# Optimization experiments

Measured on AMD Instinct MI355X. Metric: run time of the kernel, lower is better.

The kernel has to match this reference:

```python
import jax, jax.numpy as jnp
import numpy as np

B, S, D, H = 2, 2048, 1024, 16
DK = D // H


def setup_inputs() -> dict:
    key = jax.random.key(0)
    ks = jax.random.split(key, 12)
    std = 1.0 / np.sqrt(D)
    inp = {
        "query": jax.random.normal(ks[0], (B, S, D), jnp.float32),
        "key": jax.random.normal(ks[1], (B, S, D), jnp.float32),
        "value": jax.random.normal(ks[2], (B, S, D), jnp.float32),
        # causal mask: 1 = keep, 0 = blocked (matches masked_fill(mask==0, -inf))
        "mask": jnp.tril(jnp.ones((S, S), jnp.int32))[None, None, :, :],
        # torch Linear convention: W is (out, in), y = x @ W.T + b
        "Wq": jax.random.normal(ks[3], (D, D), jnp.float32) * std,
        "bq": jax.random.normal(ks[4], (D,), jnp.float32) * std,
        "Wk": jax.random.normal(ks[5], (D, D), jnp.float32) * std,
        "bk": jax.random.normal(ks[6], (D,), jnp.float32) * std,
        "Wv": jax.random.normal(ks[7], (D, D), jnp.float32) * std,
        "bv": jax.random.normal(ks[8], (D,), jnp.float32) * std,
        "Wo": jax.random.normal(ks[9], (D, D), jnp.float32) * std,
        "bo": jax.random.normal(ks[10], (D,), jnp.float32) * std,
    }
    return inp


def reference(query, key, value, mask, Wq, bq, Wk, bk, Wv, bv, Wo, bo):
    b = query.shape[0]
    # projections (torch Linear: x @ W.T + b)
    Q = query @ Wq.T + bq
    K = key @ Wk.T + bk
    V = value @ Wv.T + bv
    # (b, s, d) -> (b, h, s, dk)
    Q = Q.reshape(b, -1, H, DK).transpose(0, 2, 1, 3)
    K = K.reshape(b, -1, H, DK).transpose(0, 2, 1, 3)
    V = V.reshape(b, -1, H, DK).transpose(0, 2, 1, 3)
    scores = jnp.einsum("bhqd,bhkd->bhqk", Q, K) / jnp.sqrt(jnp.float32(DK))
    scores = jnp.where(mask == 0, -jnp.inf, scores)
    weights = jax.nn.softmax(scores, axis=-1)  # dropout p=0.0 / eval mode: no-op
    attn = jnp.einsum("bhqk,bhkd->bhqd", weights, V)
    attn = attn.transpose(0, 2, 1, 3).reshape(b, -1, D)
    return attn @ Wo.T + bo
```

## Files before the change

kernel.cpp:

```cpp
#include <hip/hip_runtime.h>
#include <hip/hip_bf16.h>
#include <cstdint>
#include <cstddef>


#define B_ 2
#define S_ 2048
#define D_ 1024
#define H_ 16
#define DK_ 64
#define QSCALE 0.1803368801111244f

typedef __attribute__((ext_vector_type(8))) short bf16x8;
typedef __attribute__((ext_vector_type(4))) float f32x4;
typedef __attribute__((ext_vector_type(16))) float f32x16;
typedef __attribute__((ext_vector_type(4))) unsigned short u16x4;
typedef __attribute__((ext_vector_type(4))) float float4v;
typedef __attribute__((ext_vector_type(2))) unsigned int u32x2;
typedef __attribute__((ext_vector_type(4))) unsigned int u32x4;

__device__ __forceinline__ unsigned short f2bf(float f) {
  unsigned int u = __float_as_uint(f);
  u += 0x7FFFu + ((u >> 16) & 1u);
  return (unsigned short)(u >> 16);
}
__device__ __forceinline__ unsigned int cvt_pk_bf16(float lo, float hi) {
  unsigned int r;
  asm("v_cvt_pk_bf16_f32 %0, %1, %2" : "=v"(r) : "v"(lo), "v"(hi));
  return r;
}
__device__ __forceinline__ bf16x8 lds_read_sw64(const unsigned short* base, int row, int col) {
  int P = (row * 64 + col) * 2;
  int X = P ^ ((row & 7) << 4);
  return *(const bf16x8*)((const char*)base + X);
}

__global__ __launch_bounds__(256) void cvt3(const float* __restrict__ s0,
                                            const float* __restrict__ s1,
                                            const float* __restrict__ s2,
                                            unsigned short* __restrict__ d0,
                                            unsigned short* __restrict__ d1,
                                            unsigned short* __restrict__ d2) {
  const float* src = blockIdx.y == 0 ? s0 : blockIdx.y == 1 ? s1 : s2;
  unsigned short* dst = blockIdx.y == 0 ? d0 : blockIdx.y == 1 ? d1 : d2;
  int i = blockIdx.x * 256 + threadIdx.x;
  float4v v = *(const float4v*)(src + (size_t)i * 4);
  u16x4 o;
  o[0] = f2bf(v[0]); o[1] = f2bf(v[1]); o[2] = f2bf(v[2]); o[3] = f2bf(v[3]);
  *(u16x4*)(dst + (size_t)i * 4) = o;
}

__global__ __launch_bounds__(256) void cvt4(const float* __restrict__ s0,
                                            const float* __restrict__ s1,
                                            const float* __restrict__ s2,
                                            const float* __restrict__ s3,
                                            unsigned short* __restrict__ d0,
                                            unsigned short* __restrict__ d1,
                                            unsigned short* __restrict__ d2,
                                            unsigned short* __restrict__ d3) {
  int z = blockIdx.y;
  const float* src = z == 0 ? s0 : z == 1 ? s1 : z == 2 ? s2 : s3;
  unsigned short* dst = z == 0 ? d0 : z == 1 ? d1 : z == 2 ? d2 : d3;
  int i = blockIdx.x * 256 + threadIdx.x;
  float4v v = *(const float4v*)(src + (size_t)i * 4);
  u16x4 o;
  o[0] = f2bf(v[0]); o[1] = f2bf(v[1]); o[2] = f2bf(v[2]); o[3] = f2bf(v[3]);
  *(u16x4*)(dst + (size_t)i * 4) = o;
}

__global__ __launch_bounds__(256) void gemm_qkv(
    const unsigned short* __restrict__ Xq, const unsigned short* __restrict__ Xk,
    const unsigned short* __restrict__ Xv, const unsigned short* __restrict__ Wq,
    const unsigned short* __restrict__ Wk, const unsigned short* __restrict__ Wv,
    const float* __restrict__ bq, const float* __restrict__ bk,
    const float* __restrict__ bv, unsigned short* __restrict__ Qp,
    unsigned short* __restrict__ Kp, unsigned short* __restrict__ Vt) {
  const int z = blockIdx.z;
  const unsigned short* A = z == 0 ? Xq : z == 1 ? Xk : Xv;
  const unsigned short* W = z == 0 ? Wq : z == 1 ? Wk : Wv;
  const float* bias = z == 0 ? bq : z == 1 ? bk : bv;
  const int K = D_, N = D_;

  __shared__ __align__(16) unsigned short As[128 * 64];
  __shared__ __align__(16) unsigned short Bs[128 * 64];
  const int tid  = threadIdx.x;
  const int lane = tid & 63;
  const int m0 = blockIdx.x * 128;
  const int n0 = blockIdx.y * 128;
  const int wr = ((tid >> 6) >> 1) * 64;
  const int wc = ((tid >> 6) & 1) * 64;
  const int lr = lane & 15;
  const int lk = (lane >> 4) * 8;
  f32x4 acc[4][4] = {};

  int dstX[4], srow[4], scolu[4];
#pragma unroll
  for (int i = 0; i < 4; ++i) {
    int X = tid * 16 + i * 4096;
    int P = X ^ (((X >> 7) & 7) << 4);
    dstX[i] = X;
    srow[i] = P >> 7;
    scolu[i] = (P & 127) >> 1;
  }

  for (int k0 = 0; k0 < K; k0 += 64) {
    __syncthreads();
#pragma unroll
    for (int i = 0; i < 4; ++i) {
      const unsigned short* gA = A + (size_t)(m0 + srow[i]) * K + k0 + scolu[i];
      const unsigned short* gB = W + (size_t)(n0 + srow[i]) * K + k0 + scolu[i];
      __builtin_amdgcn_global_load_lds((const __attribute__((address_space(1))) void*)gA,
          (__attribute__((address_space(3))) void*)((char*)As + dstX[i]), 16, 0, 0);
      __builtin_amdgcn_global_load_lds((const __attribute__((address_space(1))) void*)gB,
          (__attribute__((address_space(3))) void*)((char*)Bs + dstX[i]), 16, 0, 0);
    }
    __syncthreads();
#pragma unroll
    for (int kk = 0; kk < 2; ++kk) {
      bf16x8 a[4], b[4];
#pragma unroll
      for (int m = 0; m < 4; ++m)
        a[m] = lds_read_sw64(As, wr + m * 16 + lr, kk * 32 + lk);
#pragma unroll
      for (int n = 0; n < 4; ++n)
        b[n] = lds_read_sw64(Bs, wc + n * 16 + lr, kk * 32 + lk);
#pragma unroll
      for (int m = 0; m < 4; ++m)
#pragma unroll
        for (int n = 0; n < 4; ++n)
          acc[m][n] = __builtin_amdgcn_mfma_f32_16x16x32_bf16(a[m], b[n], acc[m][n], 0, 0, 0);
    }
  }

  const int rbase = (lane >> 4) * 4;
  if (z == 2) {
#pragma unroll
    for (int m = 0; m < 4; ++m)
#pragma unroll
      for (int n = 0; n < 4; ++n) {
        int col = n0 + wc + n * 16 + lr;
        float bvv = bias[col];
        int row0 = m0 + wr + m * 16 + rbase;
        int bb = row0 >> 11, s = row0 & 2047;
        int h = col >> 6, dk = col & 63;
        u16x4 o;
#pragma unroll
        for (int r = 0; r < 4; ++r) o[r] = f2bf(acc[m][n][r] + bvv);
        size_t idx = (((size_t)bb * H_ + h) * DK_ + dk) * S_ + s;
        *(u16x4*)(Vt + idx) = o;
      }
  } else {
    unsigned short* Cout = z == 0 ? Qp : Kp;
    const float scale = z == 0 ? QSCALE : 1.0f;
#pragma unroll
    for (int m = 0; m < 4; ++m)
#pragma unroll
      for (int n = 0; n < 4; ++n) {
        int col = n0 + wc + n * 16 + lr;
        float bvv = bias[col];
#pragma unroll
        for (int r = 0; r < 4; ++r) {
          int row = m0 + wr + m * 16 + rbase + r;
          Cout[(size_t)row * N + col] = f2bf((acc[m][n][r] + bvv) * scale);
        }
      }
  }
}

__global__ __launch_bounds__(256) void gemm_o(const unsigned short* __restrict__ A,
                                              const unsigned short* __restrict__ W,
                                              const float* __restrict__ bias,
                                              float* __restrict__ C,
                                              int M, int N, int K) {
  __shared__ __align__(16) unsigned short As[64 * 64];
  __shared__ __align__(16) unsigned short Bs[128 * 64];
  const int tid  = threadIdx.x;
  const int lane = tid & 63;
  const int m0 = blockIdx.x * 64;
  const int n0 = blockIdx.y * 128;
  const int wr = ((tid >> 6) >> 1) * 32;
  const int wc = ((tid >> 6) & 1) * 64;
  const int lr = lane & 15;
  const int lk = (lane >> 4) * 8;
  f32x4 acc[2][4] = {};

  int dstX[4], srow[4], scolu[4];
#pragma unroll
  for (int i = 0; i < 4; ++i) {
    int X = tid * 16 + i * 4096;
    int P = X ^ (((X >> 7) & 7) << 4);
    dstX[i] = X;
    srow[i] = P >> 7;
    scolu[i] = (P & 127) >> 1;
  }

  for (int k0 = 0; k0 < K; k0 += 64) {
    __syncthreads();
#pragma unroll
    for (int i = 0; i < 2; ++i) {
      const unsigned short* gA = A + (size_t)(m0 + srow[i]) * K + k0 + scolu[i];
      __builtin_amdgcn_global_load_lds((const __attribute__((address_space(1))) void*)gA,
          (__attribute__((address_space(3))) void*)((char*)As + dstX[i]), 16, 0, 0);
    }
#pragma unroll
    for (int i = 0; i < 4; ++i) {
      const unsigned short* gB = W + (size_t)(n0 + srow[i]) * K + k0 + scolu[i];
      __builtin_amdgcn_global_load_lds((const __attribute__((address_space(1))) void*)gB,
          (__attribute__((address_space(3))) void*)((char*)Bs + dstX[i]), 16, 0, 0);
    }
    __syncthreads();
#pragma unroll
    for (int kk = 0; kk < 2; ++kk) {
      bf16x8 a[2], b[4];
#pragma unroll
      for (int m = 0; m < 2; ++m)
        a[m] = lds_read_sw64(As, wr + m * 16 + lr, kk * 32 + lk);
#pragma unroll
      for (int n = 0; n < 4; ++n)
        b[n] = lds_read_sw64(Bs, wc + n * 16 + lr, kk * 32 + lk);
#pragma unroll
      for (int m = 0; m < 2; ++m)
#pragma unroll
        for (int n = 0; n < 4; ++n)
          acc[m][n] = __builtin_amdgcn_mfma_f32_16x16x32_bf16(a[m], b[n], acc[m][n], 0, 0, 0);
    }
  }

  const int rbase = (lane >> 4) * 4;
#pragma unroll
  for (int m = 0; m < 2; ++m)
#pragma unroll
    for (int n = 0; n < 4; ++n) {
      int col = n0 + wc + n * 16 + lr;
      float bvv = bias[col];
#pragma unroll
      for (int r = 0; r < 4; ++r) {
        int row = m0 + wr + m * 16 + rbase + r;
        C[(size_t)row * N + col] = acc[m][n][r] + bvv;
      }
    }
}

__device__ __forceinline__ bf16x8 lds_read_swK(const unsigned short* base, int row, int col) {
  int P = (row * 64 + col) * 2;
  int X = P ^ ((row & 7) << 4);
  return *(const bf16x8*)((const char*)base + X);
}
__device__ __forceinline__ bf16x8 lds_read_swV(const unsigned short* base, int row, int col) {
  int P = (row * 128 + col) * 2;
  int X = P ^ ((row & 7) << 4);
  return *(const bf16x8*)((const char*)base + X);
}

__global__ __launch_bounds__(512, 4) void flash_attn(const unsigned short* __restrict__ Qp,
                                                     const unsigned short* __restrict__ Kp,
                                                     const unsigned short* __restrict__ Vtp,
                                                     unsigned short* __restrict__ Op) {
  __shared__ __align__(16) unsigned short smem[32768];

  const int tid  = threadIdx.x;
  const int lane = tid & 63;
  const int w = tid >> 6;
  const int qh = w & 1;
  const int kq = w >> 1;
  const int h  = blockIdx.y;
  const int b  = blockIdx.z;
  const int ql = lane & 31;
  const int hi5 = lane >> 5;
  const size_t basebs = (size_t)b * S_ * D_;
  const int hoff = h * DK_;

  const unsigned short* gK0 = Kp + basebs + hoff;
  const unsigned short* gV0 = Vtp + ((size_t)b * H_ + h) * DK_ * S_;

  int dstXK[2], srcK[2], srcV[2];
#pragma unroll
  for (int i = 0; i < 2; ++i) {
    int X = tid * 16 + i * 8192;
    int Pk = X ^ (((X >> 7) & 7) << 4);
    dstXK[i] = X;
    srcK[i] = (Pk >> 7) * D_ + ((Pk & 127) >> 1);
    int Pv = X ^ (((X >> 8) & 7) << 4);
    srcV[i] = (Pv >> 8) * S_ + ((Pv & 255) >> 1);
  }

#define STAGE(RR, BUF)                                                         \
  {                                                                            \
    const unsigned short* gK = gK0 + (size_t)((RR) * 128) * D_;                \
    const unsigned short* gV = gV0 + (RR) * 128;                               \
    char* kb = (char*)smem + (BUF) * 32768;                                    \
    char* vb = kb + 16384;                                                     \
    _Pragma("unroll")                                                          \
    for (int i = 0; i < 2; ++i) {                                              \
      __builtin_amdgcn_global_load_lds(                                        \
          (const __attribute__((address_space(1))) void*)(gK + srcK[i]),       \
          (__attribute__((address_space(3))) void*)(kb + dstXK[i]), 16, 0, 0); \
      __builtin_amdgcn_global_load_lds(                                        \
          (const __attribute__((address_space(1))) void*)(gV + srcV[i]),       \
          (__attribute__((address_space(3))) void*)(vb + dstXK[i]), 16, 0, 0); \
    }                                                                          \
  }

  for (int s = 0; s < 2; ++s) {
    const int qt = s == 0 ? 31 - (int)blockIdx.x : (int)blockIdx.x;
    const int q0 = qt * 64;
    const int qbase = q0 + qh * 32;
    const int qglob = qbase + ql;

    bf16x8 qf[4];
    {
      const unsigned short* qrow = Qp + basebs + (size_t)qglob * D_ + hoff;
#pragma unroll
      for (int f = 0; f < 4; ++f)
        qf[f] = *(const bf16x8*)(qrow + f * 16 + hi5 * 8);
    }

    float m_r = -1e30f;
    float l_r = 0.f;
    f32x16 out0 = {};
    f32x16 out1 = {};

    const int R = (qt + 2) >> 1;

    STAGE(0, 0);
    __syncthreads();

    for (int r = 0; r < R; ++r) {
      const int cur = r & 1;
      if (r + 1 < R) STAGE(r + 1, cur ^ 1);

      const unsigned short* Kb = smem + cur * 16384;
      const unsigned short* Vb = Kb + 8192;

      const int kv0w = r * 128 + kq * 32;
      const bool act = (kv0w <= qbase);
      const bool part = (kv0w == qbase);

      if (act) {
        f32x16 sc = {};
        __builtin_amdgcn_s_setprio(1);
#pragma unroll
        for (int f = 0; f < 4; ++f) {
          bf16x8 kf = lds_read_swK(Kb, kq * 32 + ql, f * 16 + hi5 * 8);
          sc = __builtin_amdgcn_mfma_f32_32x32x16_bf16(kf, qf[f], sc, 0, 0, 0);
        }
        __builtin_amdgcn_s_setprio(0);

        if (part) {
#pragma unroll
          for (int g = 0; g < 16; ++g) {
            int kvg = kv0w + (g & 3) + 8 * (g >> 2) + 4 * hi5;
            if (kvg > qglob) sc[g] = -1e30f;
          }
        }

        float pm = sc[0];
#pragma unroll
        for (int g = 1; g < 16; ++g) pm = fmaxf(pm, sc[g]);
        pm = fmaxf(pm, __shfl_xor(pm, 32));

        if (!__all(pm - m_r <= 8.0f)) {
          float mnew = fmaxf(m_r, pm);
          float scl = __builtin_exp2f(m_r - mnew);
          l_r *= scl;
#pragma unroll
          for (int g = 0; g < 16; ++g) { out0[g] *= scl; out1[g] *= scl; }
          m_r = mnew;
        }

        float l_add = 0.f;
#define PV_CHUNK(HALF)                                                         \
        {                                                                      \
          const int g0 = (HALF) * 8;                                           \
          float p0 = __builtin_exp2f(sc[g0 + 0] - m_r);                        \
          float p1 = __builtin_exp2f(sc[g0 + 1] - m_r);                        \
          float p2 = __builtin_exp2f(sc[g0 + 2] - m_r);                        \
          float p3 = __builtin_exp2f(sc[g0 + 3] - m_r);                        \
          float p4 = __builtin_exp2f(sc[g0 + 4] - m_r);                        \
          float p5 = __builtin_exp2f(sc[g0 + 5] - m_r);                        \
          float p6 = __builtin_exp2f(sc[g0 + 6] - m_r);                        \
          float p7 = __builtin_exp2f(sc[g0 + 7] - m_r);                        \
          l_add += ((p0 + p1) + (p2 + p3)) + ((p4 + p5) + (p6 + p7));          \
          unsigned int u0 = cvt_pk_bf16(p0, p1);                               \
          unsigned int u1 = cvt_pk_bf16(p2, p3);                               \
          unsigned int u2 = cvt_pk_bf16(p4, p5);                               \
          unsigned int u3 = cvt_pk_bf16(p6, p7);                               \
          unsigned int ta = hi5 ? u0 : u2, tb = hi5 ? u1 : u3;                 \
          unsigned int ra = (unsigned int)__shfl_xor((int)ta, 32);             \
          unsigned int rb = (unsigned int)__shfl_xor((int)tb, 32);             \
          u32x4 pw = {hi5 ? ra : u0, hi5 ? rb : u1,                            \
                      hi5 ? u2 : ra, hi5 ? u3 : rb};                           \
          bf16x8 pf = __builtin_bit_cast(bf16x8, pw);                          \
          int vcol = kq * 32 + (HALF) * 16 + hi5 * 8;                          \
          bf16x8 vf0 = lds_read_swV(Vb, ql, vcol);                             \
          out0 = __builtin_amdgcn_mfma_f32_32x32x16_bf16(vf0, pf, out0, 0, 0, 0);\
          bf16x8 vf1 = lds_read_swV(Vb, 32 + ql, vcol);                       \
          out1 = __builtin_amdgcn_mfma_f32_32x32x16_bf16(vf1, pf, out1, 0, 0, 0);\
        }
        __builtin_amdgcn_s_setprio(1);
        PV_CHUNK(0);
        PV_CHUNK(1);
        __builtin_amdgcn_s_setprio(0);
#undef PV_CHUNK

        l_add += __shfl_xor(l_add, 32);
        l_r += l_add;
      }
      __syncthreads();
    }

    float* scr = (float*)smem;
    if (kq != 0) {
      float* p = scr + (((size_t)qh * 3 + (kq - 1)) * 64 + lane) * 34;
#pragma unroll
      for (int g = 0; g < 16; ++g) { p[g] = out0[g]; p[16 + g] = out1[g]; }
      p[32] = m_r;
      p[33] = l_r;
    }
    __syncthreads();
    if (kq == 0) {
      float mA = m_r, lA = l_r;
#pragma unroll
      for (int j = 0; j < 3; ++j) {
        const float* p = scr + (((size_t)qh * 3 + j) * 64 + lane) * 34;
        float mj = p[32], lj = p[33];
        float mM = fmaxf(mA, mj);
        float s0 = __builtin_exp2f(mA - mM);
        float s1 = __builtin_exp2f(mj - mM);
#pragma unroll
        for (int g = 0; g < 16; ++g) {
          out0[g] = out0[g] * s0 + p[g] * s1;
          out1[g] = out1[g] * s0 + p[16 + g] * s1;
        }
        lA = lA * s0 + lj * s1;
        mA = mM;
      }
      float rcp = 1.0f / lA;
      unsigned short* orow = Op + basebs + (size_t)qglob * D_ + hoff;
#pragma unroll
      for (int i = 0; i < 4; ++i) {
        u32x2 o0 = {cvt_pk_bf16(out0[4 * i + 0] * rcp, out0[4 * i + 1] * rcp),
                    cvt_pk_bf16(out0[4 * i + 2] * rcp, out0[4 * i + 3] * rcp)};
        *(u32x2*)(orow + 8 * i + 4 * hi5) = o0;
        u32x2 o1 = {cvt_pk_bf16(out1[4 * i + 0] * rcp, out1[4 * i + 1] * rcp),
                    cvt_pk_bf16(out1[4 * i + 2] * rcp, out1[4 * i + 3] * rcp)};
        *(u32x2*)(orow + 32 + 8 * i + 4 * hi5) = o1;
      }
    }
    __syncthreads();
  }
#undef STAGE
}

extern "C" void kernel_launch(void* const* d_in, const int* in_sizes, int n_in,
                              void* d_out, int out_size, void* d_ws, size_t ws_size,
                              hipStream_t stream) {
  const float* q  = (const float*)d_in[0];
  const float* k  = (const float*)d_in[1];
  const float* v  = (const float*)d_in[2];
  const float* Wq = (const float*)d_in[4];
  const float* bq = (const float*)d_in[5];
  const float* Wk = (const float*)d_in[6];
  const float* bk = (const float*)d_in[7];
  const float* Wv = (const float*)d_in[8];
  const float* bv = (const float*)d_in[9];
  const float* Wo = (const float*)d_in[10];
  const float* bo = (const float*)d_in[11];

  const int MSD = B_ * S_;
  unsigned short* ws = (unsigned short*)d_ws;
  unsigned short* Xq  = ws;
  unsigned short* Xk  = Xq  + (size_t)MSD * D_;
  unsigned short* Xv  = Xk  + (size_t)MSD * D_;
  unsigned short* Wqb = Xv  + (size_t)MSD * D_;
  unsigned short* Wkb = Wqb + (size_t)D_ * D_;
  unsigned short* Wvb = Wkb + (size_t)D_ * D_;
  unsigned short* Wob = Wvb + (size_t)D_ * D_;
  unsigned short* Qp  = Wob + (size_t)D_ * D_;
  unsigned short* Kp  = Qp  + (size_t)MSD * D_;
  unsigned short* Vt  = Kp  + (size_t)MSD * D_;
  unsigned short* At  = Vt  + (size_t)MSD * D_;

  const int n4a = MSD * D_ / 4;
  const int n4w = D_ * D_ / 4;
  dim3 g3(n4a / 256, 3);
  cvt3<<<g3, 256, 0, stream>>>(q, k, v, Xq, Xk, Xv);
  dim3 g4(n4w / 256, 4);
  cvt4<<<g4, 256, 0, stream>>>(Wq, Wk, Wv, Wo, Wqb, Wkb, Wvb, Wob);

  dim3 gqkv(MSD / 128, D_ / 128, 3);
  gemm_qkv<<<gqkv, 256, 0, stream>>>(Xq, Xk, Xv, Wqb, Wkb, Wvb,
                                     bq, bk, bv, Qp, Kp, Vt);

  dim3 ga(16, H_, B_);
  flash_attn<<<ga, 512, 0, stream>>>(Qp, Kp, Vt, At);

  dim3 go(MSD / 64, D_ / 128);
  gemm_o<<<go, 256, 0, stream>>>(At, Wob, bo, (float*)d_out, MSD, D_, D_);
}
```

Before: 133.2 us.

## Write Q/K/V in MFMA fragment layout and load attention operands directly to registers

The QKV projection epilogue now writes Q, K and V into a per-head fragment-ordered layout, so each lane of the attention kernel can load its MFMA operands with contiguous 16-byte global loads. The attention kernel drops LDS staging, double buffering and per-tile barriers: each of four waves walks its own strided set of 32-row KV tiles, and only the final cross-wave merge uses shared memory. Cross-half shuffles become permlane32_swap, and the grid changes to 32-query blocks of 256 threads. The risk is that K/V reuse across waves now depends on cache rather than LDS, and the Q/K epilogue writes scattered 2-byte stores.

Result: no change. 133.3 us (+0.0%).

```diff
diff --git a/kernel.cpp b/kernel.cpp
--- a/kernel.cpp
+++ b/kernel.cpp
@@ -18,6 +18,7 @@
 typedef __attribute__((ext_vector_type(4))) float float4v;
 typedef __attribute__((ext_vector_type(2))) unsigned int u32x2;
 typedef __attribute__((ext_vector_type(4))) unsigned int u32x4;
+typedef __attribute__((ext_vector_type(2))) int i32x2;
 
 __device__ __forceinline__ unsigned short f2bf(float f) {
   unsigned int u = __float_as_uint(f);
@@ -28,6 +29,15 @@
   unsigned int r;
   asm("v_cvt_pk_bf16_f32 %0, %1, %2" : "=v"(r) : "v"(lo), "v"(hi));
   return r;
+}
+__device__ __forceinline__ float partner32f(float x, int hi5) {
+  int xi = __float_as_int(x);
+  i32x2 r = __builtin_amdgcn_permlane32_swap(xi, xi, false, false);
+  return __int_as_float(hi5 ? r[0] : r[1]);
+}
+__device__ __forceinline__ unsigned int partner32u(unsigned int x, int hi5) {
+  i32x2 r = __builtin_amdgcn_permlane32_swap((int)x, (int)x, false, false);
+  return (unsigned int)(hi5 ? r[0] : r[1]);
 }
 __device__ __forceinline__ bf16x8 lds_read_sw64(const unsigned short* base, int row, int col) {
   int P = (row * 64 + col) * 2;
@@ -73,13 +83,13 @@
     const unsigned short* __restrict__ Xv, const unsigned short* __restrict__ Wq,
     const unsigned short* __restrict__ Wk, const unsigned short* __restrict__ Wv,
     const float* __restrict__ bq, const float* __restrict__ bk,
-    const float* __restrict__ bv, unsigned short* __restrict__ Qp,
-    unsigned short* __restrict__ Kp, unsigned short* __restrict__ Vt) {
+    const float* __restrict__ bv, unsigned short* __restrict__ Qf,
+    unsigned short* __restrict__ Kf, unsigned short* __restrict__ Vf) {
   const int z = blockIdx.z;
   const unsigned short* A = z == 0 ? Xq : z == 1 ? Xk : Xv;
   const unsigned short* W = z == 0 ? Wq : z == 1 ? Wk : Wv;
   const float* bias = z == 0 ? bq : z == 1 ? bk : bv;
-  const int K = D_, N = D_;
+  const int K = D_;
 
   __shared__ __align__(16) unsigned short As[128 * 64];
   __shared__ __align__(16) unsigned short Bs[128 * 64];
@@ -141,16 +151,19 @@
         int col = n0 + wc + n * 16 + lr;
         float bvv = bias[col];
         int row0 = m0 + wr + m * 16 + rbase;
-        int bb = row0 >> 11, s = row0 & 2047;
+        int bb = row0 >> 11, sr = row0 & 2047;
         int h = col >> 6, dk = col & 63;
+        int kv32 = sr >> 5, half = (sr >> 4) & 1, hi5p = (sr >> 3) & 1, e0 = sr & 7;
+        int dt = dk >> 5, qlp = dk & 31;
         u16x4 o;
 #pragma unroll
         for (int r = 0; r < 4; ++r) o[r] = f2bf(acc[m][n][r] + bvv);
-        size_t idx = (((size_t)bb * H_ + h) * DK_ + dk) * S_ + s;
-        *(u16x4*)(Vt + idx) = o;
+        size_t idx = ((((size_t)(bb * H_ + h) * 64 + kv32) * 2 + dt) * 2 + half) * 512
+                     + (hi5p * 32 + qlp) * 8 + e0;
+        *(u16x4*)(Vf + idx) = o;
       }
   } else {
-    unsigned short* Cout = z == 0 ? Qp : Kp;
+    unsigned short* Cout = z == 0 ? Qf : Kf;
     const float scale = z == 0 ? QSCALE : 1.0f;
 #pragma unroll
     for (int m = 0; m < 4; ++m)
@@ -158,11 +171,16 @@
       for (int n = 0; n < 4; ++n) {
         int col = n0 + wc + n * 16 + lr;
         float bvv = bias[col];
-#pragma unroll
-        for (int r = 0; r < 4; ++r) {
-          int row = m0 + wr + m * 16 + rbase + r;
-          Cout[(size_t)row * N + col] = f2bf((acc[m][n][r] + bvv) * scale);
-        }
+        int h = col >> 6, dk = col & 63;
+        int f = dk >> 4, hi5p = (dk >> 3) & 1, e = dk & 7;
+        int row0 = m0 + wr + m * 16 + rbase;
+        int bb = row0 >> 11, sr = row0 & 2047;
+        int s32 = sr >> 5, qlp = sr & 31;
+        size_t base = (((size_t)(bb * H_ + h) * 64 + s32) * 4 + f) * 512
+                      + (hi5p * 32 + qlp) * 8 + e;
+#pragma unroll
+        for (int r = 0; r < 4; ++r)
+          Cout[base + (size_t)r * 8] = f2bf((acc[m][n][r] + bvv) * scale);
       }
   }
 }
@@ -241,78 +259,38 @@
     }
 }
 
-__device__ __forceinline__ bf16x8 lds_read_swK(const unsigned short* base, int row, int col) {
-  int P = (row * 64 + col) * 2;
-  int X = P ^ ((row & 7) << 4);
-  return *(const bf16x8*)((const char*)base + X);
-}
-__device__ __forceinline__ bf16x8 lds_read_swV(const unsigned short* base, int row, int col) {
-  int P = (row * 128 + col) * 2;
-  int X = P ^ ((row & 7) << 4);
-  return *(const bf16x8*)((const char*)base + X);
-}
-
-__global__ __launch_bounds__(512, 4) void flash_attn(const unsigned short* __restrict__ Qp,
-                                                     const unsigned short* __restrict__ Kp,
-                                                     const unsigned short* __restrict__ Vtp,
-                                                     unsigned short* __restrict__ Op) {
-  __shared__ __align__(16) unsigned short smem[32768];
+__global__ __launch_bounds__(256, 4) void flash_reg(const unsigned short* __restrict__ Qf,
+                                                    const unsigned short* __restrict__ Kf,
+                                                    const unsigned short* __restrict__ Vf,
+                                                    unsigned short* __restrict__ Op) {
+  __shared__ float scr[3 * 64 * 34];
 
   const int tid  = threadIdx.x;
   const int lane = tid & 63;
-  const int w = tid >> 6;
-  const int qh = w & 1;
-  const int kq = w >> 1;
+  const int kq   = tid >> 6;
+  const int bx = blockIdx.x;
   const int h  = blockIdx.y;
   const int b  = blockIdx.z;
   const int ql = lane & 31;
   const int hi5 = lane >> 5;
+  const int bh = b * H_ + h;
   const size_t basebs = (size_t)b * S_ * D_;
   const int hoff = h * DK_;
 
-  const unsigned short* gK0 = Kp + basebs + hoff;
-  const unsigned short* gV0 = Vtp + ((size_t)b * H_ + h) * DK_ * S_;
-
-  int dstXK[2], srcK[2], srcV[2];
-#pragma unroll
-  for (int i = 0; i < 2; ++i) {
-    int X = tid * 16 + i * 8192;
-    int Pk = X ^ (((X >> 7) & 7) << 4);
-    dstXK[i] = X;
-    srcK[i] = (Pk >> 7) * D_ + ((Pk & 127) >> 1);
-    int Pv = X ^ (((X >> 8) & 7) << 4);
-    srcV[i] = (Pv >> 8) * S_ + ((Pv & 255) >> 1);
-  }
-
-#define STAGE(RR, BUF)                                                         \
-  {                                                                            \
-    const unsigned short* gK = gK0 + (size_t)((RR) * 128) * D_;                \
-    const unsigned short* gV = gV0 + (RR) * 128;                               \
-    char* kb = (char*)smem + (BUF) * 32768;                                    \
-    char* vb = kb + 16384;                                                     \
-    _Pragma("unroll")                                                          \
-    for (int i = 0; i < 2; ++i) {                                              \
-      __builtin_amdgcn_global_load_lds(                                        \
-          (const __attribute__((address_space(1))) void*)(gK + srcK[i]),       \
-          (__attribute__((address_space(3))) void*)(kb + dstXK[i]), 16, 0, 0); \
-      __builtin_amdgcn_global_load_lds(                                        \
-          (const __attribute__((address_space(1))) void*)(gV + srcV[i]),       \
-          (__attribute__((address_space(3))) void*)(vb + dstXK[i]), 16, 0, 0); \
-    }                                                                          \
-  }
+  const unsigned short* Qb = Qf + (size_t)bh * 131072 + lane * 8;
+  const unsigned short* Kb = Kf + (size_t)bh * 131072 + lane * 8;
+  const unsigned short* Vb = Vf + (size_t)bh * 131072 + lane * 8;
 
   for (int s = 0; s < 2; ++s) {
-    const int qt = s == 0 ? 31 - (int)blockIdx.x : (int)blockIdx.x;
-    const int q0 = qt * 64;
-    const int qbase = q0 + qh * 32;
-    const int qglob = qbase + ql;
-
-    bf16x8 qf[4];
+    const int j = s == 0 ? 63 - bx : bx;
+    const int q0 = j * 32;
+    const int qglob = q0 + ql;
+
+    bf16x8 qf4[4];
     {
-      const unsigned short* qrow = Qp + basebs + (size_t)qglob * D_ + hoff;
-#pragma unroll
-      for (int f = 0; f < 4; ++f)
-        qf[f] = *(const bf16x8*)(qrow + f * 16 + hi5 * 8);
+      const unsigned short* qp_ = Qb + (size_t)j * 2048;
+#pragma unroll
+      for (int f = 0; f < 4; ++f) qf4[f] = *(const bf16x8*)(qp_ + f * 512);
     }
 
     float m_r = -1e30f;
@@ -320,98 +298,88 @@
     f32x16 out0 = {};
     f32x16 out1 = {};
 
-    const int R = (qt + 2) >> 1;
-
-    STAGE(0, 0);
-    __syncthreads();
-
-    for (int r = 0; r < R; ++r) {
-      const int cur = r & 1;
-      if (r + 1 < R) STAGE(r + 1, cur ^ 1);
-
-      const unsigned short* Kb = smem + cur * 16384;
-      const unsigned short* Vb = Kb + 8192;
-
-      const int kv0w = r * 128 + kq * 32;
-      const bool act = (kv0w <= qbase);
-      const bool part = (kv0w == qbase);
-
-      if (act) {
-        f32x16 sc = {};
-        __builtin_amdgcn_s_setprio(1);
-#pragma unroll
-        for (int f = 0; f < 4; ++f) {
-          bf16x8 kf = lds_read_swK(Kb, kq * 32 + ql, f * 16 + hi5 * 8);
-          sc = __builtin_amdgcn_mfma_f32_32x32x16_bf16(kf, qf[f], sc, 0, 0, 0);
+    for (int w = kq; w <= j; w += 4) {
+      const unsigned short* kp_ = Kb + (size_t)w * 2048;
+      bf16x8 kf0 = *(const bf16x8*)(kp_);
+      bf16x8 kf1 = *(const bf16x8*)(kp_ + 512);
+      bf16x8 kf2 = *(const bf16x8*)(kp_ + 1024);
+      bf16x8 kf3 = *(const bf16x8*)(kp_ + 1536);
+
+      f32x16 sc = {};
+      __builtin_amdgcn_s_setprio(1);
+      sc = __builtin_amdgcn_mfma_f32_32x32x16_bf16(kf0, qf4[0], sc, 0, 0, 0);
+      sc = __builtin_amdgcn_mfma_f32_32x32x16_bf16(kf1, qf4[1], sc, 0, 0, 0);
+      sc = __builtin_amdgcn_mfma_f32_32x32x16_bf16(kf2, qf4[2], sc, 0, 0, 0);
+      sc = __builtin_amdgcn_mfma_f32_32x32x16_bf16(kf3, qf4[3], sc, 0, 0, 0);
+      __builtin_amdgcn_s_setprio(0);
+
+      const unsigned short* vp_ = Vb + (size_t)w * 2048;
+      bf16x8 vf00 = *(const bf16x8*)(vp_);
+      bf16x8 vf01 = *(const bf16x8*)(vp_ + 512);
+      bf16x8 vf10 = *(const bf16x8*)(vp_ + 1024);
+      bf16x8 vf11 = *(const bf16x8*)(vp_ + 1536);
+
+      if (w == j) {
+#pragma unroll
+        for (int g = 0; g < 16; ++g) {
+          int kvg = w * 32 + (g & 3) + 8 * (g >> 2) + 4 * hi5;
+          if (kvg > qglob) sc[g] = -1e30f;
         }
-        __builtin_amdgcn_s_setprio(0);
-
-        if (part) {
-#pragma unroll
-          for (int g = 0; g < 16; ++g) {
-            int kvg = kv0w + (g & 3) + 8 * (g >> 2) + 4 * hi5;
-            if (kvg > qglob) sc[g] = -1e30f;
-          }
-        }
-
-        float pm = sc[0];
-#pragma unroll
-        for (int g = 1; g < 16; ++g) pm = fmaxf(pm, sc[g]);
-        pm = fmaxf(pm, __shfl_xor(pm, 32));
-
-        if (!__all(pm - m_r <= 8.0f)) {
-          float mnew = fmaxf(m_r, pm);
-          float scl = __builtin_exp2f(m_r - mnew);
-          l_r *= scl;
-#pragma unroll
-          for (int g = 0; g < 16; ++g) { out0[g] *= scl; out1[g] *= scl; }
-          m_r = mnew;
-        }
-
-        float l_add = 0.f;
-#define PV_CHUNK(HALF)                                                         \
-        {                                                                      \
-          const int g0 = (HALF) * 8;                                           \
-          float p0 = __builtin_exp2f(sc[g0 + 0] - m_r);                        \
-          float p1 = __builtin_exp2f(sc[g0 + 1] - m_r);                        \
-          float p2 = __builtin_exp2f(sc[g0 + 2] - m_r);                        \
-          float p3 = __builtin_exp2f(sc[g0 + 3] - m_r);                        \
-          float p4 = __builtin_exp2f(sc[g0 + 4] - m_r);                        \
-          float p5 = __builtin_exp2f(sc[g0 + 5] - m_r);                        \
-          float p6 = __builtin_exp2f(sc[g0 + 6] - m_r);                        \
-          float p7 = __builtin_exp2f(sc[g0 + 7] - m_r);                        \
-          l_add += ((p0 + p1) + (p2 + p3)) + ((p4 + p5) + (p6 + p7));          \
-          unsigned int u0 = cvt_pk_bf16(p0, p1);                               \
-          unsigned int u1 = cvt_pk_bf16(p2, p3);                               \
-          unsigned int u2 = cvt_pk_bf16(p4, p5);                               \
-          unsigned int u3 = cvt_pk_bf16(p6, p7);                               \
-          unsigned int ta = hi5 ? u0 : u2, tb = hi5 ? u1 : u3;                 \
-          unsigned int ra = (unsigned int)__shfl_xor((int)ta, 32);             \
-          unsigned int rb = (unsigned int)__shfl_xor((int)tb, 32);             \
-          u32x4 pw = {hi5 ? ra : u0, hi5 ? rb : u1,                            \
-                      hi5 ? u2 : ra, hi5 ? u3 : rb};                           \
-          bf16x8 pf = __builtin_bit_cast(bf16x8, pw);                          \
-          int vcol = kq * 32 + (HALF) * 16 + hi5 * 8;                          \
-          bf16x8 vf0 = lds_read_swV(Vb, ql, vcol);                             \
-          out0 = __builtin_amdgcn_mfma_f32_32x32x16_bf16(vf0, pf, out0, 0, 0, 0);\
-          bf16x8 vf1 = lds_read_swV(Vb, 32 + ql, vcol);                       \
-          out1 = __builtin_amdgcn_mfma_f32_32x32x16_bf16(vf1, pf, out1, 0, 0, 0);\
-        }
-        __builtin_amdgcn_s_setprio(1);
-        PV_CHUNK(0);
-        PV_CHUNK(1);
-        __builtin_amdgcn_s_setprio(0);
-#undef PV_CHUNK
-
-        l_add += __shfl_xor(l_add, 32);
-        l_r += l_add;
-      }
-      __syncthreads();
-    }
-
-    float* scr = (float*)smem;
+      }
+
+      float pm = sc[0];
+#pragma unroll
+      for (int g = 1; g < 16; ++g) pm = fmaxf(pm, sc[g]);
+      pm = fmaxf(pm, partner32f(pm, hi5));
+
+      if (!__all(pm - m_r <= 8.0f)) {
+        float mnew = fmaxf(m_r, pm);
+        float scl = __builtin_exp2f(m_r - mnew);
+        l_r *= scl;
+#pragma unroll
+        for (int g = 0; g < 16; ++g) { out0[g] *= scl; out1[g] *= scl; }
+        m_r = mnew;
+      }
+
+      float l_add = 0.f;
+#define PV_HALF(HALF, VF0, VF1)                                                \
+      {                                                                        \
+        const int g0 = (HALF) * 8;                                             \
+        float p0 = __builtin_exp2f(sc[g0 + 0] - m_r);                          \
+        float p1 = __builtin_exp2f(sc[g0 + 1] - m_r);                          \
+        float p2 = __builtin_exp2f(sc[g0 + 2] - m_r);                          \
+        float p3 = __builtin_exp2f(sc[g0 + 3] - m_r);                          \
+        float p4 = __builtin_exp2f(sc[g0 + 4] - m_r);                          \
+        float p5 = __builtin_exp2f(sc[g0 + 5] - m_r);                          \
+        float p6 = __builtin_exp2f(sc[g0 + 6] - m_r);                          \
+        float p7 = __builtin_exp2f(sc[g0 + 7] - m_r);                          \
+        l_add += ((p0 + p1) + (p2 + p3)) + ((p4 + p5) + (p6 + p7));            \
+        unsigned int u0 = cvt_pk_bf16(p0, p1);                                 \
+        unsigned int u1 = cvt_pk_bf16(p2, p3);                                 \
+        unsigned int u2 = cvt_pk_bf16(p4, p5);                                 \
+        unsigned int u3 = cvt_pk_bf16(p6, p7);                                 \
+        unsigned int ta = hi5 ? u0 : u2, tb = hi5 ? u1 : u3;                   \
+        unsigned int ra = partner32u(ta, hi5);                                 \
+        unsigned int rb = partner32u(tb, hi5);                                 \
+        u32x4 pw = {hi5 ? ra : u0, hi5 ? rb : u1,                              \
+                    hi5 ? u2 : ra, hi5 ? u3 : rb};                             \
+        bf16x8 pf = __builtin_bit_cast(bf16x8, pw);                            \
+        out0 = __builtin_amdgcn_mfma_f32_32x32x16_bf16(VF0, pf, out0, 0, 0, 0);\
+        out1 = __builtin_amdgcn_mfma_f32_32x32x16_bf16(VF1, pf, out1, 0, 0, 0);\
+      }
+      __builtin_amdgcn_s_setprio(1);
+      PV_HALF(0, vf00, vf10);
+      PV_HALF(1, vf01, vf11);
+      __builtin_amdgcn_s_setprio(0);
+#undef PV_HALF
+
+      l_add += partner32f(l_add, hi5);
+      l_r += l_add;
+    }
+
+    __syncthreads();
     if (kq != 0) {
-      float* p = scr + (((size_t)qh * 3 + (kq - 1)) * 64 + lane) * 34;
+      float* p = scr + ((size_t)(kq - 1) * 64 + lane) * 34;
 #pragma unroll
       for (int g = 0; g < 16; ++g) { p[g] = out0[g]; p[16 + g] = out1[g]; }
       p[32] = m_r;
@@ -421,8 +389,8 @@
     if (kq == 0) {
       float mA = m_r, lA = l_r;
 #pragma unroll
-      for (int j = 0; j < 3; ++j) {
-        const float* p = scr + (((size_t)qh * 3 + j) * 64 + lane) * 34;
+      for (int j3 = 0; j3 < 3; ++j3) {
+        const float* p = scr + ((size_t)j3 * 64 + lane) * 34;
         float mj = p[32], lj = p[33];
         float mM = fmaxf(mA, mj);
         float s0 = __builtin_exp2f(mA - mM);
@@ -449,7 +417,6 @@
     }
     __syncthreads();
   }
-#undef STAGE
 }
 
 extern "C" void kernel_launch(void* const* d_in, const int* in_sizes, int n_in,
@@ -476,10 +443,10 @@
   unsigned short* Wkb = Wqb + (size_t)D_ * D_;
   unsigned short* Wvb = Wkb + (size_t)D_ * D_;
   unsigned short* Wob = Wvb + (size_t)D_ * D_;
-  unsigned short* Qp  = Wob + (size_t)D_ * D_;
-  unsigned short* Kp  = Qp  + (size_t)MSD * D_;
-  unsigned short* Vt  = Kp  + (size_t)MSD * D_;
-  unsigned short* At  = Vt  + (size_t)MSD * D_;
+  unsigned short* Qf  = Wob + (size_t)D_ * D_;
+  unsigned short* Kf  = Qf  + (size_t)MSD * D_;
+  unsigned short* Vf  = Kf  + (size_t)MSD * D_;
+  unsigned short* At  = Vf  + (size_t)MSD * D_;
 
   const int n4a = MSD * D_ / 4;
   const int n4w = D_ * D_ / 4;
@@ -490,10 +457,10 @@
 
   dim3 gqkv(MSD / 128, D_ / 128, 3);
   gemm_qkv<<<gqkv, 256, 0, stream>>>(Xq, Xk, Xv, Wqb, Wkb, Wvb,
-                                     bq, bk, bv, Qp, Kp, Vt);
-
-  dim3 ga(16, H_, B_);
-  flash_attn<<<ga, 512, 0, stream>>>(Qp, Kp, Vt, At);
+                                     bq, bk, bv, Qf, Kf, Vf);
+
+  dim3 ga(32, H_, B_);
+  flash_reg<<<ga, 256, 0, stream>>>(Qf, Kf, Vf, At);
 
   dim3 go(MSD / 64, D_ / 128);
   gemm_o<<<go, 256, 0, stream>>>(At, Wob, bo, (float*)d_out, MSD, D_, D_);
```
